# Kernel optimization log

Measured on AMD Instinct MI355X. Metric: run time of the kernel, lower is better.

Reference implementation:

```python
import jax, jax.numpy as jnp
import numpy as np

B, N, D, E = 4, 256, 256, 256


def setup_inputs() -> dict:
    key = jax.random.key(0)
    ks = jax.random.split(key, 8)
    nrm = lambda k, shape, sc=1.0: (jax.random.normal(k, shape, dtype=jnp.float32) * sc)
    nodes = nrm(ks[0], (B, N, D))
    edges = nrm(ks[1], (B, N, N, E))
    auxiliary_matrix = nrm(ks[2], (B, N, N, 1))
    # Linear params (PyTorch Linear: y = x @ W.T + b; here stored pre-transposed as [in, out])
    W_in = nrm(ks[3], (2 * D + E, D), (2 * D + E) ** -0.5)
    b_in = jnp.zeros((D,), jnp.float32)
    W_coef = nrm(ks[4], (D, 1), D ** -0.5)
    b_coef = jnp.zeros((1,), jnp.float32)
    W_out = nrm(ks[5], (D, D), D ** -0.5)
    b_out = jnp.zeros((D,), jnp.float32)
    return {
        'nodes': nodes, 'edges': edges, 'auxiliary_matrix': auxiliary_matrix,
        'nums': N,
        'W_in': W_in, 'b_in': b_in, 'W_coef': W_coef, 'b_coef': b_coef,
        'W_out': W_out, 'b_out': b_out,
    }


def reference(nodes, edges, auxiliary_matrix, nums, W_in, b_in, W_coef, b_coef, W_out, b_out):
    b, n, d = nodes.shape
    # pairwise start/end node features (original multiplies by a ones tensor; pure broadcast here)
    start = jnp.broadcast_to(nodes[:, :, None, :], (b, n, n, d))
    end = jnp.broadcast_to(nodes[:, None, :, :], (b, n, n, d))
    cat_nodes = jnp.concatenate([start, end, edges], axis=-1)          # [B,N,N,2D+E]
    cat_nodes = jax.nn.relu(cat_nodes @ W_in + b_in)                   # [B,N,N,D]
    coefs = cat_nodes @ W_coef + b_coef                                # [B,N,N,1]
    attn = jax.nn.softmax(auxiliary_matrix + coefs, axis=2)            # softmax over neighbor dim
    # permute((0,1,3,2)).sum(3) == sum over axis 2
    residuals = jnp.sum(attn * cat_nodes, axis=2)                      # [B,N,D]
    nodes_out = nodes + jax.nn.relu(residuals @ W_out + b_out)
    return (nodes_out, cat_nodes)
```

## Files before the change

kernel.cpp:

```cpp
#include <hip/hip_runtime.h>
#include <cstdint>
#include <cstddef>


typedef float f32x4 __attribute__((ext_vector_type(4)));
typedef __bf16 bf16x8 __attribute__((ext_vector_type(8)));

#define AS1 __attribute__((address_space(1)))
#define AS3 __attribute__((address_space(3)))

__device__ __forceinline__ void async_cp16(const void* g, void* l) {
  __builtin_amdgcn_global_load_lds((const AS1 void*)g, (AS3 void*)l, 16, 0, 0);
}

__global__ __launch_bounds__(256) void k_pack(const float* __restrict__ W_in,
                                              __bf16* __restrict__ W_p) {
  int idx = blockIdx.x * 256 + threadIdx.x;
  int kb8 = idx >> 8;
  int c = idx & 255;
  bf16x8 v;
#pragma unroll
  for (int e = 0; e < 8; ++e) v[e] = (__bf16)W_in[(size_t)(512 + kb8 * 8 + e) * 256 + c];
  *reinterpret_cast<bf16x8*>(W_p + (size_t)idx * 8) = v;
}

__global__ __launch_bounds__(256) void k_ac(const float* __restrict__ nodes,
                                            const float* __restrict__ W_in,
                                            const float* __restrict__ b_in,
                                            float* __restrict__ A, float* __restrict__ C) {
  __shared__ float nd[4][256];
  const int t = threadIdx.x;
  const int row0 = blockIdx.x * 4;
#pragma unroll
  for (int r = 0; r < 4; ++r) nd[r][t] = nodes[(size_t)(row0 + r) * 256 + t];
  __syncthreads();
  float accA[4] = {0.f, 0.f, 0.f, 0.f}, accC[4] = {0.f, 0.f, 0.f, 0.f};
#pragma unroll 4
  for (int k = 0; k < 256; ++k) {
    float ws_ = W_in[(size_t)k * 256 + t];
    float we_ = W_in[(size_t)(256 + k) * 256 + t];
#pragma unroll
    for (int r = 0; r < 4; ++r) {
      accA[r] += nd[r][k] * ws_;
      accC[r] += nd[r][k] * we_;
    }
  }
  float bi = b_in[t];
#pragma unroll
  for (int r = 0; r < 4; ++r) {
    A[(size_t)(row0 + r) * 256 + t] = accA[r] + bi;
    C[(size_t)(row0 + r) * 256 + t] = accC[r];
  }
}

__global__ __launch_bounds__(256, 2) void k_main(
    const float* __restrict__ edges, const float* __restrict__ aux,
    const float* __restrict__ A, const float* __restrict__ C,
    const __bf16* __restrict__ W_p, const float* __restrict__ W_coef,
    const float* __restrict__ b_coef, float* __restrict__ out_cat,
    float* __restrict__ resid) {
  __shared__ float ET[64 * 256];
  __shared__ float coef_l[64];
  __shared__ float w_lds[64];

  const int tid = threadIdx.x;
  const int lane = tid & 63;
  const int wv = tid >> 6;
  const int l15 = lane & 15;
  const int lg = lane >> 4;
  const int bi = blockIdx.x;
  const int b = bi >> 8;

  const f32x4 vzero = {0.f, 0.f, 0.f, 0.f};

  float pA[4], wc[4];
#pragma unroll
  for (int nc = 0; nc < 4; ++nc) {
    int d = wv * 64 + nc * 16 + l15;
    pA[nc] = A[(size_t)bi * 256 + d];
    wc[nc] = W_coef[d];
  }
  const float bcoef = b_coef[0];

  const float* eg_base = edges + (size_t)bi * (256 * 256);
  float* cat_base = out_cat + (size_t)bi * (256 * 256);

  float m_run = -INFINITY, l_run = 0.f;
  float r_lane[4] = {0.f, 0.f, 0.f, 0.f};
  f32x4 acc[4][4];

  for (int jt = 0; jt < 4; ++jt) {
    const int j0 = jt * 64;
    if (tid < 64) coef_l[tid] = 0.f;

    {
      const char* gB = (const char*)(eg_base + (size_t)j0 * 256);
#pragma unroll
      for (int it = 0; it < 16; ++it) {
        int q = it * 256 + tid;
        int row = q >> 6, cc = q & 63;
        int gchunk = (row << 6) | (cc ^ (row & 7));
        char* dst = (char*)ET + (size_t)(it * 256 + (tid & ~63)) * 16;
        async_cp16(gB + (size_t)gchunk * 16, dst);
      }
    }
    asm volatile("s_waitcnt vmcnt(0)" ::: "memory");
    __syncthreads();

#pragma unroll
    for (int mr = 0; mr < 4; ++mr)
#pragma unroll
      for (int nc = 0; nc < 4; ++nc) acc[mr][nc] = vzero;

    const f32x4* ET4 = (const f32x4*)ET;
#pragma unroll 1
    for (int ks = 0; ks < 8; ++ks) {
      bf16x8 bfr[4];
#pragma unroll
      for (int nc = 0; nc < 4; ++nc) {
        int col = wv * 64 + nc * 16 + l15;
        int kb8 = ks * 4 + lg;
        bfr[nc] = *reinterpret_cast<const bf16x8*>(W_p + ((size_t)kb8 * 256 + col) * 8);
      }
#pragma unroll
      for (int mr = 0; mr < 4; ++mr) {
        int arow = mr * 16 + l15;
        int kc = ks * 8 + lg * 2;
        int sw = arow & 7;
        f32x4 fa = ET4[arow * 64 + (kc ^ sw)];
        f32x4 fb = ET4[arow * 64 + ((kc + 1) ^ sw)];
        bf16x8 af;
#pragma unroll
        for (int e = 0; e < 4; ++e) {
          af[e] = (__bf16)fa[e];
          af[4 + e] = (__bf16)fb[e];
        }
#pragma unroll
        for (int nc = 0; nc < 4; ++nc)
          acc[mr][nc] = __builtin_amdgcn_mfma_f32_16x16x32_bf16(af, bfr[nc], acc[mr][nc], 0, 0, 0);
      }
    }

#pragma unroll
    for (int mr = 0; mr < 4; ++mr) {
#pragma unroll
      for (int r = 0; r < 4; ++r) {
        int jl = mr * 16 + lg * 4 + r;
        int j = j0 + jl;
        const float* Crow = C + ((size_t)(b * 256 + j)) * 256;
        float cp = 0.f;
#pragma unroll
        for (int nc = 0; nc < 4; ++nc) {
          int d = wv * 64 + nc * 16 + l15;
          float pre = acc[mr][nc][r] + pA[nc] + Crow[d];
          float cv = fmaxf(pre, 0.f);
          acc[mr][nc][r] = cv;
          cat_base[(size_t)j * 256 + d] = cv;
          cp += cv * wc[nc];
        }
        cp += __shfl_xor(cp, 1);
        cp += __shfl_xor(cp, 2);
        cp += __shfl_xor(cp, 4);
        cp += __shfl_xor(cp, 8);
        if (l15 == 0) atomicAdd(&coef_l[jl], cp);
      }
    }
    __syncthreads();

    float sc = coef_l[lane] + aux[(size_t)bi * 256 + j0 + lane] + bcoef;
    float mt = sc;
#pragma unroll
    for (int mm = 1; mm < 64; mm <<= 1) mt = fmaxf(mt, __shfl_xor(mt, mm));
    float mnew = fmaxf(m_run, mt);
    float scalef = __expf(m_run - mnew);
    float wgt = __expf(sc - mnew);
    float st = wgt;
#pragma unroll
    for (int mm = 1; mm < 64; mm <<= 1) st += __shfl_xor(st, mm);
    l_run = l_run * scalef + st;
    m_run = mnew;
    if (tid < 64) w_lds[tid] = wgt;
    __syncthreads();

#pragma unroll
    for (int nc = 0; nc < 4; ++nc) r_lane[nc] *= scalef;
#pragma unroll
    for (int mr = 0; mr < 4; ++mr) {
#pragma unroll
      for (int r = 0; r < 4; ++r) {
        float wj = w_lds[mr * 16 + lg * 4 + r];
#pragma unroll
        for (int nc = 0; nc < 4; ++nc) r_lane[nc] += wj * acc[mr][nc][r];
      }
    }
  }

#pragma unroll
  for (int nc = 0; nc < 4; ++nc) {
    float r = r_lane[nc];
    r += __shfl_xor(r, 16);
    r += __shfl_xor(r, 32);
    if (lg == 0) resid[(size_t)bi * 256 + wv * 64 + nc * 16 + l15] = r / l_run;
  }
}

__global__ __launch_bounds__(256) void k_out(const float* __restrict__ nodes,
                                             const float* __restrict__ resid,
                                             const float* __restrict__ W_out,
                                             const float* __restrict__ b_out,
                                             float* __restrict__ out_nodes) {
  __shared__ float rs[4][256];
  const int t = threadIdx.x;
  const int row0 = blockIdx.x * 4;
#pragma unroll
  for (int r = 0; r < 4; ++r) rs[r][t] = resid[(size_t)(row0 + r) * 256 + t];
  __syncthreads();
  float acc[4] = {0.f, 0.f, 0.f, 0.f};
#pragma unroll 4
  for (int k = 0; k < 256; ++k) {
    float wv_ = W_out[(size_t)k * 256 + t];
#pragma unroll
    for (int r = 0; r < 4; ++r) acc[r] += rs[r][k] * wv_;
  }
  float bo = b_out[t];
#pragma unroll
  for (int r = 0; r < 4; ++r) {
    out_nodes[(size_t)(row0 + r) * 256 + t] =
        nodes[(size_t)(row0 + r) * 256 + t] + fmaxf(acc[r] + bo, 0.f);
  }
}

extern "C" void kernel_launch(void* const* d_in, const int* in_sizes, int n_in,
                              void* d_out, int out_size, void* d_ws, size_t ws_size,
                              hipStream_t stream) {
  const float* nodes = (const float*)d_in[0];
  const float* edges = (const float*)d_in[1];
  const float* aux = (const float*)d_in[2];
  const float* W_in = (const float*)d_in[4];
  const float* b_in = (const float*)d_in[5];
  const float* W_coef = (const float*)d_in[6];
  const float* b_coef = (const float*)d_in[7];
  const float* W_out = (const float*)d_in[8];
  const float* b_out = (const float*)d_in[9];

  float* out_nodes = (float*)d_out;
  float* out_cat = out_nodes + 4 * 256 * 256;

  float* A = (float*)d_ws;
  float* Cm = A + 4 * 256 * 256;
  float* resid = Cm + 4 * 256 * 256;
  __bf16* W_p = (__bf16*)(resid + 4 * 256 * 256);

  k_pack<<<dim3(32), dim3(256), 0, stream>>>(W_in, W_p);
  k_ac<<<dim3(256), dim3(256), 0, stream>>>(nodes, W_in, b_in, A, Cm);
  k_main<<<dim3(1024), dim3(256), 0, stream>>>(edges, aux, A, Cm, W_p, W_coef, b_coef,
                                               out_cat, resid);
  k_out<<<dim3(256), dim3(256), 0, stream>>>(nodes, resid, W_out, b_out, out_nodes);
}
```

Before: 598.5 us.

## Double-buffer bf16 edge tiles in LDS with register-staged prefetch in k_main

Replaces the synchronous fp32 global-to-LDS copy of 64-row edge tiles with 32-row tiles. Each tile is loaded into registers, converted to bf16 once and written to a double-buffered swizzled LDS area, so loads for the next tile overlap the MFMA and epilogue of the current one. The smaller LDS footprint allows 4 blocks per CU instead of 2. It also removes the LDS atomics for the coefficient reduction in favour of per-wave slots, and broadcasts softmax weights by shuffle instead of through LDS, saving one barrier per tile. The cost is more loop iterations, register pressure from 8 staged vectors under a tighter launch bound, and possible spills.

```diff
diff --git a/kernel.cpp b/kernel.cpp
--- a/kernel.cpp
+++ b/kernel.cpp
@@ -4,14 +4,8 @@
 
 
 typedef float f32x4 __attribute__((ext_vector_type(4)));
+typedef __bf16 bf16x4 __attribute__((ext_vector_type(4)));
 typedef __bf16 bf16x8 __attribute__((ext_vector_type(8)));
-
-#define AS1 __attribute__((address_space(1)))
-#define AS3 __attribute__((address_space(3)))
-
-__device__ __forceinline__ void async_cp16(const void* g, void* l) {
-  __builtin_amdgcn_global_load_lds((const AS1 void*)g, (AS3 void*)l, 16, 0, 0);
-}
 
 __global__ __launch_bounds__(256) void k_pack(const float* __restrict__ W_in,
                                               __bf16* __restrict__ W_p) {
@@ -53,15 +47,14 @@
   }
 }
 
-__global__ __launch_bounds__(256, 2) void k_main(
+__global__ __launch_bounds__(256, 4) void k_main(
     const float* __restrict__ edges, const float* __restrict__ aux,
     const float* __restrict__ A, const float* __restrict__ C,
     const __bf16* __restrict__ W_p, const float* __restrict__ W_coef,
     const float* __restrict__ b_coef, float* __restrict__ out_cat,
     float* __restrict__ resid) {
-  __shared__ float ET[64 * 256];
-  __shared__ float coef_l[64];
-  __shared__ float w_lds[64];
+  __shared__ __bf16 ET[2][32 * 256];
+  __shared__ float coefw[2][4][32];
 
   const int tid = threadIdx.x;
   const int lane = tid & 63;
@@ -82,67 +75,77 @@
   }
   const float bcoef = b_coef[0];
 
-  const float* eg_base = edges + (size_t)bi * (256 * 256);
-  float* cat_base = out_cat + (size_t)bi * (256 * 256);
+  const float* eg = edges + (size_t)bi * 65536;
+  float* catb = out_cat + (size_t)bi * 65536;
 
   float m_run = -INFINITY, l_run = 0.f;
   float r_lane[4] = {0.f, 0.f, 0.f, 0.f};
-  f32x4 acc[4][4];
-
-  for (int jt = 0; jt < 4; ++jt) {
-    const int j0 = jt * 64;
-    if (tid < 64) coef_l[tid] = 0.f;
-
-    {
-      const char* gB = (const char*)(eg_base + (size_t)j0 * 256);
-#pragma unroll
-      for (int it = 0; it < 16; ++it) {
-        int q = it * 256 + tid;
-        int row = q >> 6, cc = q & 63;
-        int gchunk = (row << 6) | (cc ^ (row & 7));
-        char* dst = (char*)ET + (size_t)(it * 256 + (tid & ~63)) * 16;
-        async_cp16(gB + (size_t)gchunk * 16, dst);
-      }
-    }
-    asm volatile("s_waitcnt vmcnt(0)" ::: "memory");
-    __syncthreads();
-
-#pragma unroll
-    for (int mr = 0; mr < 4; ++mr)
+
+  f32x4 R[8];
+
+#define STAGE_LOAD(J0, IT) \
+  R[IT] = *reinterpret_cast<const f32x4*>(eg + (size_t)((J0) + (IT)*4 + wv) * 256 + (lane << 2));
+
+#define STAGE_WRITE(BUF, IT)                                                         \
+  {                                                                                  \
+    int row_ = (IT)*4 + wv;                                                          \
+    int slot_ = ((lane >> 1) ^ (row_ & 7));                                          \
+    __bf16* p_ = &ET[BUF][row_ * 256] + slot_ * 8 + (lane & 1) * 4;                  \
+    bf16x4 v_;                                                                       \
+    v_[0] = (__bf16)R[IT][0]; v_[1] = (__bf16)R[IT][1];                              \
+    v_[2] = (__bf16)R[IT][2]; v_[3] = (__bf16)R[IT][3];                              \
+    *reinterpret_cast<bf16x4*>(p_) = v_;                                             \
+  }
+
+#pragma unroll
+  for (int it = 0; it < 8; ++it) STAGE_LOAD(0, it)
+#pragma unroll
+  for (int it = 0; it < 8; ++it) STAGE_WRITE(0, it)
+  __syncthreads();
+
+  f32x4 acc[2][4];
+
+#pragma unroll 1
+  for (int jt = 0; jt < 8; ++jt) {
+    const int buf = jt & 1;
+    const int j0 = jt * 32;
+
+    if (jt < 7) {
+#pragma unroll
+      for (int it = 0; it < 4; ++it) STAGE_LOAD(j0 + 32, it)
+    }
+
+#pragma unroll
+    for (int mr = 0; mr < 2; ++mr)
 #pragma unroll
       for (int nc = 0; nc < 4; ++nc) acc[mr][nc] = vzero;
 
-    const f32x4* ET4 = (const f32x4*)ET;
-#pragma unroll 1
+#pragma unroll
     for (int ks = 0; ks < 8; ++ks) {
-      bf16x8 bfr[4];
+      bf16x8 af[2];
+#pragma unroll
+      for (int mr = 0; mr < 2; ++mr) {
+        int arow = mr * 16 + l15;
+        int slotp = ((ks << 2) | lg) ^ (arow & 7);
+        af[mr] = *reinterpret_cast<const bf16x8*>(&ET[buf][arow * 256] + slotp * 8);
+      }
 #pragma unroll
       for (int nc = 0; nc < 4; ++nc) {
         int col = wv * 64 + nc * 16 + l15;
-        int kb8 = ks * 4 + lg;
-        bfr[nc] = *reinterpret_cast<const bf16x8*>(W_p + ((size_t)kb8 * 256 + col) * 8);
-      }
-#pragma unroll
-      for (int mr = 0; mr < 4; ++mr) {
-        int arow = mr * 16 + l15;
-        int kc = ks * 8 + lg * 2;
-        int sw = arow & 7;
-        f32x4 fa = ET4[arow * 64 + (kc ^ sw)];
-        f32x4 fb = ET4[arow * 64 + ((kc + 1) ^ sw)];
-        bf16x8 af;
-#pragma unroll
-        for (int e = 0; e < 4; ++e) {
-          af[e] = (__bf16)fa[e];
-          af[4 + e] = (__bf16)fb[e];
-        }
-#pragma unroll
-        for (int nc = 0; nc < 4; ++nc)
-          acc[mr][nc] = __builtin_amdgcn_mfma_f32_16x16x32_bf16(af, bfr[nc], acc[mr][nc], 0, 0, 0);
-      }
-    }
-
-#pragma unroll
-    for (int mr = 0; mr < 4; ++mr) {
+        bf16x8 bw = *reinterpret_cast<const bf16x8*>(
+            W_p + (((size_t)((ks << 2) | lg) * 256 + col) << 3));
+        acc[0][nc] = __builtin_amdgcn_mfma_f32_16x16x32_bf16(af[0], bw, acc[0][nc], 0, 0, 0);
+        acc[1][nc] = __builtin_amdgcn_mfma_f32_16x16x32_bf16(af[1], bw, acc[1][nc], 0, 0, 0);
+      }
+    }
+
+    if (jt < 7) {
+#pragma unroll
+      for (int it = 4; it < 8; ++it) STAGE_LOAD(j0 + 32, it)
+    }
+
+#pragma unroll
+    for (int mr = 0; mr < 2; ++mr) {
 #pragma unroll
       for (int r = 0; r < 4; ++r) {
         int jl = mr * 16 + lg * 4 + r;
@@ -152,56 +155,64 @@
 #pragma unroll
         for (int nc = 0; nc < 4; ++nc) {
           int d = wv * 64 + nc * 16 + l15;
-          float pre = acc[mr][nc][r] + pA[nc] + Crow[d];
-          float cv = fmaxf(pre, 0.f);
+          float cv = fmaxf(acc[mr][nc][r] + pA[nc] + Crow[d], 0.f);
           acc[mr][nc][r] = cv;
-          cat_base[(size_t)j * 256 + d] = cv;
+          catb[(size_t)j * 256 + d] = cv;
           cp += cv * wc[nc];
         }
         cp += __shfl_xor(cp, 1);
         cp += __shfl_xor(cp, 2);
         cp += __shfl_xor(cp, 4);
         cp += __shfl_xor(cp, 8);
-        if (l15 == 0) atomicAdd(&coef_l[jl], cp);
-      }
-    }
+        if (l15 == 0) coefw[buf][wv][jl] = cp;
+      }
+    }
+
+    if (jt < 7) {
+#pragma unroll
+      for (int it = 0; it < 8; ++it) STAGE_WRITE(buf ^ 1, it)
+    }
+
     __syncthreads();
 
-    float sc = coef_l[lane] + aux[(size_t)bi * 256 + j0 + lane] + bcoef;
+    int jl32 = lane & 31;
+    float sc = coefw[buf][0][jl32] + coefw[buf][1][jl32] + coefw[buf][2][jl32] +
+               coefw[buf][3][jl32] + aux[(size_t)bi * 256 + j0 + jl32] + bcoef;
     float mt = sc;
 #pragma unroll
-    for (int mm = 1; mm < 64; mm <<= 1) mt = fmaxf(mt, __shfl_xor(mt, mm));
+    for (int mm = 1; mm < 32; mm <<= 1) mt = fmaxf(mt, __shfl_xor(mt, mm));
     float mnew = fmaxf(m_run, mt);
     float scalef = __expf(m_run - mnew);
     float wgt = __expf(sc - mnew);
     float st = wgt;
 #pragma unroll
-    for (int mm = 1; mm < 64; mm <<= 1) st += __shfl_xor(st, mm);
+    for (int mm = 1; mm < 32; mm <<= 1) st += __shfl_xor(st, mm);
     l_run = l_run * scalef + st;
     m_run = mnew;
-    if (tid < 64) w_lds[tid] = wgt;
-    __syncthreads();
 
 #pragma unroll
     for (int nc = 0; nc < 4; ++nc) r_lane[nc] *= scalef;
 #pragma unroll
-    for (int mr = 0; mr < 4; ++mr) {
+    for (int mr = 0; mr < 2; ++mr) {
 #pragma unroll
       for (int r = 0; r < 4; ++r) {
-        float wj = w_lds[mr * 16 + lg * 4 + r];
+        float wj = __shfl(wgt, mr * 16 + lg * 4 + r);
 #pragma unroll
         for (int nc = 0; nc < 4; ++nc) r_lane[nc] += wj * acc[mr][nc][r];
       }
     }
   }
 
+  float inv_l = 1.0f / l_run;
 #pragma unroll
   for (int nc = 0; nc < 4; ++nc) {
     float r = r_lane[nc];
     r += __shfl_xor(r, 16);
     r += __shfl_xor(r, 32);
-    if (lg == 0) resid[(size_t)bi * 256 + wv * 64 + nc * 16 + l15] = r / l_run;
-  }
+    if (lg == 0) resid[(size_t)bi * 256 + wv * 64 + nc * 16 + l15] = r * inv_l;
+  }
+#undef STAGE_LOAD
+#undef STAGE_WRITE
 }
 
 __global__ __launch_bounds__(256) void k_out(const float* __restrict__ nodes,
```

New measurement: 847.4 us. 41.6% more time.
